# Performance work log

Hardware: AMD Instinct MI355X
Metric: run time of the kernel (lower is better)

## Reference

```python
import jax, jax.numpy as jnp
import numpy as np

S_N = 100000   # number of students (embedding rows)
K_N = 30       # knowledge dim; must equal stu_dim=30 per the torch code
N_OUT = 1024   # number of exercises / output dim
B = 4096       # batch size
K_SEL = 3      # k_n_select
NVARS = 2 ** K_SEL - 2  # 6


def setup_inputs() -> dict:
    key = jax.random.key(0)
    ks = jax.random.split(key, 12)
    stu_id = jax.random.randint(ks[0], (B,), 0, S_N)
    exer_id = jax.random.randint(ks[1], (B,), 0, N_OUT)  # unused by forward, kept for fidelity
    kn_emb = jax.random.normal(ks[2], (B, K_N), jnp.float32)  # unused by forward
    # q matrix: exactly 3 ones per row -> sorted column indices (matches boolean-mask gather order)
    rng = np.random.default_rng(0)
    q_idx = np.stack([np.sort(rng.choice(K_N, K_SEL, replace=False)) for _ in range(N_OUT)])
    q_idx = jnp.asarray(q_idx, dtype=jnp.int32)  # [N_OUT, 3]
    emb = jax.random.normal(ks[3], (S_N, 30), jnp.float32) * 0.05
    fm_vars = jnp.abs(jax.random.normal(ks[4], (NVARS, N_OUT), jnp.float32)) * 0.1 + (1.0 / K_SEL)
    def lin(k, fan_out, fan_in):
        std = (2.0 / (fan_in + fan_out)) ** 0.5  # xavier normal
        return jax.random.normal(k, (fan_out, fan_in), jnp.float32) * std
    w1 = lin(ks[5], 256, N_OUT); b1 = jnp.zeros((256,), jnp.float32)
    w2 = lin(ks[6], 128, 256);   b2 = jnp.zeros((128,), jnp.float32)
    w3 = lin(ks[7], N_OUT, 128); b3 = jnp.zeros((N_OUT,), jnp.float32)
    return {"stu_id": stu_id, "exer_id": exer_id, "kn_emb": kn_emb, "q_idx": q_idx,
            "emb": emb, "fm_vars": fm_vars,
            "w1": w1, "b1": b1, "w2": w2, "b2": b2, "w3": w3, "b3": b3}


def _chi_fm(fm_vars):
    # fuzzy-measure construction for k_n_select=3 (subset lattice hardcoded, matches torch loop)
    chi = jnp.abs(fm_vars)            # [6, N_OUT]
    f0, f1 = chi[0], chi[1]
    f2 = jnp.maximum(f0, f1) + chi[2]
    f3 = chi[3]
    f4 = jnp.maximum(f3, f0) + chi[4]
    f5 = jnp.maximum(f3, f1) + chi[5]
    FM = jnp.stack([f0, f1, f2, f3, f4, f5, jnp.ones_like(f0)], axis=0)  # [7, N_OUT]
    return jnp.minimum(FM, 1.0).T     # [N_OUT, 7]


def reference(stu_id, exer_id, kn_emb, q_idx, emb, fm_vars, w1, b1, w2, b2, w3, b3):
    stu = jnp.take(emb, stu_id, axis=0)          # [B, 30]
    sel = jax.nn.sigmoid(stu)                     # [B, K_N]
    inputs = sel[:, q_idx]                        # gather -> [B, N_OUT, 3]
    idx = jnp.argsort(-inputs, axis=2)            # descending sort indices
    sv = jnp.take_along_axis(inputs, idx, axis=2) # sorted values, descending
    # diff with trailing zero: sv[k] - sv[k+1]
    diffs = sv - jnp.concatenate([sv[:, :, 1:], jnp.zeros_like(sv[:, :, :1])], axis=2)
    out_idx = jnp.cumsum(2 ** idx, axis=2) - 1    # subset node index in [0, 6], distinct per row
    bI = jnp.arange(inputs.shape[0])[:, None, None]
    nI = jnp.arange(inputs.shape[1])[None, :, None]
    alpha = jnp.zeros(inputs.shape[:2] + (NVARS + 1,), sv.dtype).at[bI, nI, out_idx].set(diffs)
    FM = _chi_fm(fm_vars)                          # [N_OUT, 7]
    C = jnp.sum(alpha * FM[None], axis=2)          # Choquet integral [B, N_OUT]
    h = jax.nn.relu(C @ w1.T + b1)                 # dropout is identity in eval
    h = jax.nn.relu(h @ w2.T + b2)
    return jax.nn.sigmoid(h @ w3.T + b3)           # [B, N_OUT]
```

## Files before the change

### kernel.cpp

```cpp
#include <hip/hip_runtime.h>
#include <math.h>

#define K_N   30
#define N_OUT 1024
#define BB    4096
#define SMEM_BYTES 81920

typedef unsigned short ushort_t;
typedef __attribute__((ext_vector_type(8))) short bf16x8;
typedef __attribute__((ext_vector_type(4))) float f32x4;

#define MFMA(a, b, c) (c) = __builtin_amdgcn_mfma_f32_16x16x32_bf16((a), (b), (c), 0, 0, 0)

__device__ __forceinline__ ushort_t f2bf(float x) {
  union { float f; unsigned u; } a; a.f = x;
  unsigned r = a.u + 0x7FFFu + ((a.u >> 16) & 1u);
  return (ushort_t)(r >> 16);
}
__device__ __forceinline__ float bf2f(ushort_t h) {
  union { float f; unsigned u; } a; a.u = ((unsigned)h) << 16;
  return a.f;
}

__device__ __forceinline__ float choquet_one(float v0, float v1, float v2,
                                             float F0, float F1, float F2,
                                             float F3, float F4, float F5) {
  bool c01 = v1 > v0, c02 = v2 > v0, c12 = v2 > v1;
  int r0 = (int)c01 + (int)c02;
  int r1 = (int)(!c01) + (int)c12;
  int p0 = (r0 == 0) ? 0 : ((r1 == 0) ? 1 : 2);
  int p1 = (r0 == 1) ? 0 : ((r1 == 1) ? 1 : 2);
  int p2 = 3 - p0 - p1;
  float sv0 = (p0 == 0) ? v0 : ((p0 == 1) ? v1 : v2);
  float sv1 = (p1 == 0) ? v0 : ((p1 == 1) ? v1 : v2);
  float sv2 = (p2 == 0) ? v0 : ((p2 == 1) ? v1 : v2);
  float fm0 = (p0 == 0) ? F0 : ((p0 == 1) ? F1 : F3);
  float fm1 = (p2 == 2) ? F2 : ((p2 == 1) ? F4 : F5);
  return (sv0 - sv1) * fm0 + (sv1 - sv2) * fm1 + sv2;
}

__global__ __launch_bounds__(512) void cicdm_split(
    const float* __restrict__ w1, const float* __restrict__ w2,
    const float* __restrict__ w3, ushort_t* __restrict__ w1fh,
    ushort_t* __restrict__ w1fl, ushort_t* __restrict__ w2fh,
    ushort_t* __restrict__ w2fl, ushort_t* __restrict__ w3fh,
    ushort_t* __restrict__ w3fl) {
  int i = blockIdx.x * 512 + threadIdx.x;
  float v;
  ushort_t *ph, *pl;
  int dst;
  if (i < 262144) {
    int c = i >> 10, k = i & 1023;
    v = w1[i];
    dst = ((c >> 4) * 32 + (k >> 5)) * 512 + (((k >> 3) & 3) * 16 + (c & 15)) * 8 + (k & 7);
    ph = w1fh; pl = w1fl;
  } else if (i < 294912) {
    int i2 = i - 262144;
    int c = i2 >> 8, k = i2 & 255;
    v = w2[i2];
    dst = ((c >> 4) * 8 + (k >> 5)) * 512 + (((k >> 3) & 3) * 16 + (c & 15)) * 8 + (k & 7);
    ph = w2fh; pl = w2fl;
  } else {
    int i3 = i - 294912;
    int c = i3 >> 7, k = i3 & 127;
    v = w3[i3];
    dst = ((c >> 4) * 4 + (k >> 5)) * 512 + (((k >> 3) & 3) * 16 + (c & 15)) * 8 + (k & 7);
    ph = w3fh; pl = w3fl;
  }
  ushort_t h = f2bf(v);
  ph[dst] = h;
  pl[dst] = f2bf(v - bf2f(h));
}

__global__ __launch_bounds__(512, 2) void cicdm_fused(
    const int* __restrict__ stu_id, const int* __restrict__ q_idx,
    const float* __restrict__ emb, const float* __restrict__ fm_vars,
    const float* __restrict__ b1, const float* __restrict__ b2,
    const float* __restrict__ b3, const ushort_t* __restrict__ w1fh,
    const ushort_t* __restrict__ w1fl, const ushort_t* __restrict__ w2fh,
    const ushort_t* __restrict__ w2fl, const ushort_t* __restrict__ w3fh,
    const ushort_t* __restrict__ w3fl, float* __restrict__ out) {
  extern __shared__ __align__(16) char dsm[];
  ushort_t* sC = (ushort_t*)dsm;
  float* sSel = (float*)(dsm + 65536);
  ushort_t* sH1 = (ushort_t*)(dsm + 65536);
  ushort_t* sH2 = (ushort_t*)dsm;

  const int bid = blockIdx.x, tid = threadIdx.x;
  const int lane = tid & 63, wid = tid >> 6;
  const int lrow = lane & 15, lc = lane >> 4;
  const int row0 = bid * 16;

  if (tid < 16 * K_N) {
    int r = tid / K_N, c = tid % K_N;
    float x = emb[(size_t)stu_id[row0 + r] * K_N + c];
    sSel[r * 32 + c] = 1.f / (1.f + expf(-x));
  }
  __syncthreads();
  {
    const int n0 = tid * 2;
    const int qa0 = q_idx[n0 * 3 + 0], qa1 = q_idx[n0 * 3 + 1],
              qa2 = q_idx[n0 * 3 + 2];
    const int qb0 = q_idx[n0 * 3 + 3], qb1 = q_idx[n0 * 3 + 4],
              qb2 = q_idx[n0 * 3 + 5];
    float fa[6], fb[6];
#pragma unroll
    for (int v = 0; v < 6; ++v) {
      fa[v] = fabsf(fm_vars[v * N_OUT + n0]);
      fb[v] = fabsf(fm_vars[v * N_OUT + n0 + 1]);
    }
    float A0 = fminf(fa[0], 1.f), A1 = fminf(fa[1], 1.f), A3 = fminf(fa[3], 1.f);
    float A2 = fminf(fmaxf(fa[0], fa[1]) + fa[2], 1.f);
    float A4 = fminf(fmaxf(fa[3], fa[0]) + fa[4], 1.f);
    float A5 = fminf(fmaxf(fa[3], fa[1]) + fa[5], 1.f);
    float B0 = fminf(fb[0], 1.f), B1 = fminf(fb[1], 1.f), B3 = fminf(fb[3], 1.f);
    float B2 = fminf(fmaxf(fb[0], fb[1]) + fb[2], 1.f);
    float B4 = fminf(fmaxf(fb[3], fb[0]) + fb[4], 1.f);
    float B5 = fminf(fmaxf(fb[3], fb[1]) + fb[5], 1.f);
    const int kc = n0 >> 3, wi = n0 & 7;
#pragma unroll 4
    for (int r = 0; r < 16; ++r) {
      const float* sr = sSel + r * 32;
      float cA = choquet_one(sr[qa0], sr[qa1], sr[qa2], A0, A1, A2, A3, A4, A5);
      float cB = choquet_one(sr[qb0], sr[qb1], sr[qb2], B0, B1, B2, B3, B4, B5);
      ushort_t hA = f2bf(cA), hB = f2bf(cB);
      ushort_t lA = f2bf(cA - bf2f(hA)), lB = f2bf(cB - bf2f(hB));
      int byo = r * 2048 + ((kc ^ (r & 7)) * 8 + wi) * 2;
      *(unsigned*)((char*)sC + byo) = (unsigned)hA | ((unsigned)hB << 16);
      *(unsigned*)((char*)sC + 32768 + byo) = (unsigned)lA | ((unsigned)lB << 16);
    }
  }
  __syncthreads();

  {
    const ushort_t* baseH = w1fh + wid * 32768 + lane * 8;
    const ushort_t* baseL = w1fl + wid * 32768 + lane * 8;
    bf16x8 ph[4], pl[4];
    f32x4 cA1 = {}, cA2 = {}, cB1 = {}, cB2 = {};
    bf16x8 ah = {}, al = {};
#define LD1(s, d)                                                   \
  do {                                                              \
    int o = (((s) & 1) * 16384) + (((s) >> 1) * 512);               \
    ph[d] = *(const bf16x8*)(baseH + o);                            \
    pl[d] = *(const bf16x8*)(baseL + o);                            \
  } while (0)
    LD1(0, 0); LD1(1, 1); LD1(2, 2); LD1(3, 3);
#pragma unroll
    for (int s = 0; s < 64; ++s) {
      int kc = s >> 1;
      if ((s & 1) == 0) {
        int pA = (kc * 4 + lc) ^ (lrow & 7);
        ah = *(const bf16x8*)(sC + lrow * 1024 + pA * 8);
        al = *(const bf16x8*)(sC + 16384 + lrow * 1024 + pA * 8);
      }
      bf16x8 wh = ph[s & 3], wl = pl[s & 3];
      if ((s & 1) == 0) {
        MFMA(ah, wh, cA1); MFMA(ah, wl, cA2); MFMA(al, wh, cA2);
      } else {
        MFMA(ah, wh, cB1); MFMA(ah, wl, cB2); MFMA(al, wh, cB2);
      }
      if (s + 4 < 64) LD1(s + 4, s & 3);
    }
#undef LD1
    f32x4 accs[2] = {cA1 + cA2, cB1 + cB2};
#pragma unroll
    for (int j = 0; j < 2; ++j) {
      int col = wid * 32 + j * 16 + lrow;
      float bv = b1[col];
      int kc2 = col >> 3, wi2 = col & 7;
#pragma unroll
      for (int rr = 0; rr < 4; ++rr) {
        int r = lc * 4 + rr;
        float v = fmaxf(accs[j][rr] + bv, 0.f);
        ushort_t h = f2bf(v);
        int byo = r * 512 + ((kc2 ^ (r & 7)) * 8 + wi2) * 2;
        *(ushort_t*)((char*)sH1 + byo) = h;
        *(ushort_t*)((char*)sH1 + 8192 + byo) = f2bf(v - bf2f(h));
      }
    }
  }
  __syncthreads();

  {
    const ushort_t* baseH = w2fh + wid * 4096 + lane * 8;
    const ushort_t* baseL = w2fl + wid * 4096 + lane * 8;
    bf16x8 ph[4], pl[4];
    f32x4 c1 = {}, c2 = {};
#define LD2(s, d)                                                   \
  do {                                                              \
    int o = (s) * 512;                                              \
    ph[d] = *(const bf16x8*)(baseH + o);                            \
    pl[d] = *(const bf16x8*)(baseL + o);                            \
  } while (0)
    LD2(0, 0); LD2(1, 1); LD2(2, 2); LD2(3, 3);
#pragma unroll
    for (int s = 0; s < 8; ++s) {
      int pA = (s * 4 + lc) ^ (lrow & 7);
      bf16x8 ah = *(const bf16x8*)(sH1 + lrow * 256 + pA * 8);
      bf16x8 al = *(const bf16x8*)(sH1 + 4096 + lrow * 256 + pA * 8);
      bf16x8 wh = ph[s & 3], wl = pl[s & 3];
      MFMA(ah, wh, c1); MFMA(ah, wl, c2); MFMA(al, wh, c2);
      if (s + 4 < 8) LD2(s + 4, s & 3);
    }
#undef LD2
    f32x4 acc = c1 + c2;
    int col = wid * 16 + lrow;
    float bv = b2[col];
    int kc2 = col >> 3, wi2 = col & 7;
#pragma unroll
    for (int rr = 0; rr < 4; ++rr) {
      int r = lc * 4 + rr;
      float v = fmaxf(acc[rr] + bv, 0.f);
      ushort_t h = f2bf(v);
      int byo = r * 256 + ((kc2 ^ (r & 7)) * 8 + wi2) * 2;
      *(ushort_t*)((char*)sH2 + byo) = h;
      *(ushort_t*)((char*)sH2 + 4096 + byo) = f2bf(v - bf2f(h));
    }
  }
  __syncthreads();

  {
    const ushort_t* baseH = w3fh + wid * 16384 + lane * 8;
    const ushort_t* baseL = w3fl + wid * 16384 + lane * 8;
    bf16x8 ph[4], pl[4];
    f32x4 a1[8] = {}, a2[8] = {};
    bf16x8 ah = {}, al = {};
#define LD3(s, d)                                                   \
  do {                                                              \
    int o = (((s) & 7) * 2048) + (((s) >> 3) * 512);                \
    ph[d] = *(const bf16x8*)(baseH + o);                            \
    pl[d] = *(const bf16x8*)(baseL + o);                            \
  } while (0)
    LD3(0, 0); LD3(1, 1); LD3(2, 2); LD3(3, 3);
#pragma unroll
    for (int s = 0; s < 32; ++s) {
      int ks = s >> 3, cg = s & 7;
      if (cg == 0) {
        int pA = (ks * 4 + lc) ^ (lrow & 7);
        ah = *(const bf16x8*)(sH2 + lrow * 128 + pA * 8);
        al = *(const bf16x8*)(sH2 + 2048 + lrow * 128 + pA * 8);
      }
      bf16x8 wh = ph[s & 3], wl = pl[s & 3];
      MFMA(ah, wh, a1[cg]); MFMA(ah, wl, a2[cg]); MFMA(al, wh, a2[cg]);
      if (s + 4 < 32) LD3(s + 4, s & 3);
    }
#undef LD3
#pragma unroll
    for (int cg = 0; cg < 8; ++cg) {
      f32x4 acc = a1[cg] + a2[cg];
      int col = wid * 128 + cg * 16 + lrow;
      float bv = b3[col];
#pragma unroll
      for (int rr = 0; rr < 4; ++rr) {
        int row = row0 + lc * 4 + rr;
        float v = acc[rr] + bv;
        out[(size_t)row * N_OUT + col] = 1.f / (1.f + expf(-v));
      }
    }
  }
}

extern "C" void kernel_launch(void* const* d_in, const int* in_sizes, int n_in,
                              void* d_out, int out_size, void* d_ws,
                              size_t ws_size, hipStream_t stream) {
  const int* stu_id = (const int*)d_in[0];
  const int* q_idx = (const int*)d_in[3];
  const float* emb = (const float*)d_in[4];
  const float* fm_vars = (const float*)d_in[5];
  const float* w1 = (const float*)d_in[6];
  const float* b1 = (const float*)d_in[7];
  const float* w2 = (const float*)d_in[8];
  const float* b2 = (const float*)d_in[9];
  const float* w3 = (const float*)d_in[10];
  const float* b3 = (const float*)d_in[11];
  float* out = (float*)d_out;

  char* ws = (char*)d_ws;
  size_t off = 0;
  auto alloc = [&](size_t bytes) {
    void* p = ws + off;
    off += (bytes + 255) & ~(size_t)255;
    return p;
  };
  ushort_t* w1fh = (ushort_t*)alloc(256 * N_OUT * 2);
  ushort_t* w1fl = (ushort_t*)alloc(256 * N_OUT * 2);
  ushort_t* w2fh = (ushort_t*)alloc(128 * 256 * 2);
  ushort_t* w2fl = (ushort_t*)alloc(128 * 256 * 2);
  ushort_t* w3fh = (ushort_t*)alloc(N_OUT * 128 * 2);
  ushort_t* w3fl = (ushort_t*)alloc(N_OUT * 128 * 2);

  (void)hipFuncSetAttribute((const void*)cicdm_fused,
                            hipFuncAttributeMaxDynamicSharedMemorySize,
                            SMEM_BYTES);

  cicdm_split<<<832, 512, 0, stream>>>(w1, w2, w3, w1fh, w1fl, w2fh, w2fl,
                                       w3fh, w3fl);
  cicdm_fused<<<256, 512, SMEM_BYTES, stream>>>(stu_id, q_idx, emb, fm_vars,
                                                b1, b2, b3, w1fh, w1fl, w2fh,
                                                w2fl, w3fh, w3fl, out);
}
```

Measured before the change: 120.0 us.

## Deepen weight prefetch and overlap it across stages and the Choquet prologue

Increases the global weight-fragment prefetch depth from 4 to 8 stages per layer. The first layer's weights are now issued before the embedding gather and Choquet computation. Each later layer's weights are issued before the previous layer's epilogue and barrier, so loads overlap computation and synchronisation. It also double-buffers the LDS activation fragments so the next k-chunk is read ahead of the MFMAs. The cost is more live vector registers (16 bf16x8 prefetch registers plus A buffers) under launch_bounds(512,2), which may cause spills.

```diff
diff --git a/kernel.cpp b/kernel.cpp
--- a/kernel.cpp
+++ b/kernel.cpp
@@ -90,6 +90,38 @@
   const int lane = tid & 63, wid = tid >> 6;
   const int lrow = lane & 15, lc = lane >> 4;
   const int row0 = bid * 16;
+  const int sw = lrow & 7;
+
+  const ushort_t* w1H = w1fh + wid * 32768 + lane * 8;
+  const ushort_t* w1L = w1fl + wid * 32768 + lane * 8;
+  const ushort_t* w2H = w2fh + wid * 4096 + lane * 8;
+  const ushort_t* w2L = w2fl + wid * 4096 + lane * 8;
+  const ushort_t* w3H = w3fh + wid * 16384 + lane * 8;
+  const ushort_t* w3L = w3fl + wid * 16384 + lane * 8;
+
+  bf16x8 ph[8], pl[8];
+
+#define LD1(s, d)                                             \
+  do {                                                        \
+    int o = (((s) & 1) * 16384) + (((s) >> 1) * 512);         \
+    ph[d] = *(const bf16x8*)(w1H + o);                        \
+    pl[d] = *(const bf16x8*)(w1L + o);                        \
+  } while (0)
+#define LD2(s, d)                                             \
+  do {                                                        \
+    int o = (s) * 512;                                        \
+    ph[d] = *(const bf16x8*)(w2H + o);                        \
+    pl[d] = *(const bf16x8*)(w2L + o);                        \
+  } while (0)
+#define LD3(s, d)                                             \
+  do {                                                        \
+    int o = (((s) & 7) * 2048) + (((s) >> 3) * 512);          \
+    ph[d] = *(const bf16x8*)(w3H + o);                        \
+    pl[d] = *(const bf16x8*)(w3L + o);                        \
+  } while (0)
+
+  LD1(0, 0); LD1(1, 1); LD1(2, 2); LD1(3, 3);
+  LD1(4, 4); LD1(5, 5); LD1(6, 6); LD1(7, 7);
 
   if (tid < 16 * K_N) {
     int r = tid / K_N, c = tid % K_N;
@@ -133,35 +165,32 @@
   __syncthreads();
 
   {
-    const ushort_t* baseH = w1fh + wid * 32768 + lane * 8;
-    const ushort_t* baseL = w1fl + wid * 32768 + lane * 8;
-    bf16x8 ph[4], pl[4];
     f32x4 cA1 = {}, cA2 = {}, cB1 = {}, cB2 = {};
-    bf16x8 ah = {}, al = {};
-#define LD1(s, d)                                                   \
-  do {                                                              \
-    int o = (((s) & 1) * 16384) + (((s) >> 1) * 512);               \
-    ph[d] = *(const bf16x8*)(baseH + o);                            \
-    pl[d] = *(const bf16x8*)(baseL + o);                            \
-  } while (0)
-    LD1(0, 0); LD1(1, 1); LD1(2, 2); LD1(3, 3);
+    bf16x8 aH[2], aL[2];
+    {
+      int pA = lc ^ sw;
+      aH[0] = *(const bf16x8*)(sC + lrow * 1024 + pA * 8);
+      aL[0] = *(const bf16x8*)(sC + 16384 + lrow * 1024 + pA * 8);
+    }
 #pragma unroll
     for (int s = 0; s < 64; ++s) {
       int kc = s >> 1;
-      if ((s & 1) == 0) {
-        int pA = (kc * 4 + lc) ^ (lrow & 7);
-        ah = *(const bf16x8*)(sC + lrow * 1024 + pA * 8);
-        al = *(const bf16x8*)(sC + 16384 + lrow * 1024 + pA * 8);
-      }
-      bf16x8 wh = ph[s & 3], wl = pl[s & 3];
+      if ((s & 1) == 0 && kc + 1 < 32) {
+        int pA = ((kc + 1) * 4 + lc) ^ sw;
+        aH[(kc + 1) & 1] = *(const bf16x8*)(sC + lrow * 1024 + pA * 8);
+        aL[(kc + 1) & 1] = *(const bf16x8*)(sC + 16384 + lrow * 1024 + pA * 8);
+      }
+      bf16x8 wh = ph[s & 7], wl = pl[s & 7];
+      bf16x8 ah = aH[kc & 1], al = aL[kc & 1];
       if ((s & 1) == 0) {
         MFMA(ah, wh, cA1); MFMA(ah, wl, cA2); MFMA(al, wh, cA2);
       } else {
         MFMA(ah, wh, cB1); MFMA(ah, wl, cB2); MFMA(al, wh, cB2);
       }
-      if (s + 4 < 64) LD1(s + 4, s & 3);
-    }
-#undef LD1
+      if (s + 8 < 64) LD1(s + 8, s & 7);
+    }
+    LD2(0, 0); LD2(1, 1); LD2(2, 2); LD2(3, 3);
+    LD2(4, 4); LD2(5, 5); LD2(6, 6); LD2(7, 7);
     f32x4 accs[2] = {cA1 + cA2, cB1 + cB2};
 #pragma unroll
     for (int j = 0; j < 2; ++j) {
@@ -182,27 +211,26 @@
   __syncthreads();
 
   {
-    const ushort_t* baseH = w2fh + wid * 4096 + lane * 8;
-    const ushort_t* baseL = w2fl + wid * 4096 + lane * 8;
-    bf16x8 ph[4], pl[4];
     f32x4 c1 = {}, c2 = {};
-#define LD2(s, d)                                                   \
-  do {                                                              \
-    int o = (s) * 512;                                              \
-    ph[d] = *(const bf16x8*)(baseH + o);                            \
-    pl[d] = *(const bf16x8*)(baseL + o);                            \
-  } while (0)
-    LD2(0, 0); LD2(1, 1); LD2(2, 2); LD2(3, 3);
+    bf16x8 aH[2], aL[2];
+    {
+      int pA = lc ^ sw;
+      aH[0] = *(const bf16x8*)(sH1 + lrow * 256 + pA * 8);
+      aL[0] = *(const bf16x8*)(sH1 + 4096 + lrow * 256 + pA * 8);
+    }
 #pragma unroll
     for (int s = 0; s < 8; ++s) {
-      int pA = (s * 4 + lc) ^ (lrow & 7);
-      bf16x8 ah = *(const bf16x8*)(sH1 + lrow * 256 + pA * 8);
-      bf16x8 al = *(const bf16x8*)(sH1 + 4096 + lrow * 256 + pA * 8);
-      bf16x8 wh = ph[s & 3], wl = pl[s & 3];
-      MFMA(ah, wh, c1); MFMA(ah, wl, c2); MFMA(al, wh, c2);
-      if (s + 4 < 8) LD2(s + 4, s & 3);
-    }
-#undef LD2
+      if (s + 1 < 8) {
+        int pA = ((s + 1) * 4 + lc) ^ sw;
+        aH[(s + 1) & 1] = *(const bf16x8*)(sH1 + lrow * 256 + pA * 8);
+        aL[(s + 1) & 1] = *(const bf16x8*)(sH1 + 4096 + lrow * 256 + pA * 8);
+      }
+      MFMA(aH[s & 1], ph[s & 7], c1);
+      MFMA(aH[s & 1], pl[s & 7], c2);
+      MFMA(aL[s & 1], ph[s & 7], c2);
+    }
+    LD3(0, 0); LD3(1, 1); LD3(2, 2); LD3(3, 3);
+    LD3(4, 4); LD3(5, 5); LD3(6, 6); LD3(7, 7);
     f32x4 acc = c1 + c2;
     int col = wid * 16 + lrow;
     float bv = b2[col];
@@ -220,31 +248,26 @@
   __syncthreads();
 
   {
-    const ushort_t* baseH = w3fh + wid * 16384 + lane * 8;
-    const ushort_t* baseL = w3fl + wid * 16384 + lane * 8;
-    bf16x8 ph[4], pl[4];
     f32x4 a1[8] = {}, a2[8] = {};
-    bf16x8 ah = {}, al = {};
-#define LD3(s, d)                                                   \
-  do {                                                              \
-    int o = (((s) & 7) * 2048) + (((s) >> 3) * 512);                \
-    ph[d] = *(const bf16x8*)(baseH + o);                            \
-    pl[d] = *(const bf16x8*)(baseL + o);                            \
-  } while (0)
-    LD3(0, 0); LD3(1, 1); LD3(2, 2); LD3(3, 3);
+    bf16x8 aH[2], aL[2];
+    {
+      int pA = lc ^ sw;
+      aH[0] = *(const bf16x8*)(sH2 + lrow * 128 + pA * 8);
+      aL[0] = *(const bf16x8*)(sH2 + 2048 + lrow * 128 + pA * 8);
+    }
 #pragma unroll
     for (int s = 0; s < 32; ++s) {
       int ks = s >> 3, cg = s & 7;
-      if (cg == 0) {
-        int pA = (ks * 4 + lc) ^ (lrow & 7);
-        ah = *(const bf16x8*)(sH2 + lrow * 128 + pA * 8);
-        al = *(const bf16x8*)(sH2 + 2048 + lrow * 128 + pA * 8);
-      }
-      bf16x8 wh = ph[s & 3], wl = pl[s & 3];
-      MFMA(ah, wh, a1[cg]); MFMA(ah, wl, a2[cg]); MFMA(al, wh, a2[cg]);
-      if (s + 4 < 32) LD3(s + 4, s & 3);
-    }
-#undef LD3
+      if (cg == 0 && ks + 1 < 4) {
+        int pA = ((ks + 1) * 4 + lc) ^ sw;
+        aH[(ks + 1) & 1] = *(const bf16x8*)(sH2 + lrow * 128 + pA * 8);
+        aL[(ks + 1) & 1] = *(const bf16x8*)(sH2 + 2048 + lrow * 128 + pA * 8);
+      }
+      MFMA(aH[ks & 1], ph[s & 7], a1[cg]);
+      MFMA(aH[ks & 1], pl[s & 7], a2[cg]);
+      MFMA(aL[ks & 1], ph[s & 7], a2[cg]);
+      if (s + 8 < 32) LD3(s + 8, s & 7);
+    }
 #pragma unroll
     for (int cg = 0; cg < 8; ++cg) {
       f32x4 acc = a1[cg] + a2[cg];
@@ -258,6 +281,9 @@
       }
     }
   }
+#undef LD1
+#undef LD2
+#undef LD3
 }
 
 extern "C" void kernel_launch(void* const* d_in, const int* in_sizes, int n_in,
```

Result: faster. 116.0 us (-3.3%).
